# Optimization experiments

Measured on AMD Instinct MI355X. Metric: run time of the kernel, lower is better.

Reference implementation:

```python
import jax, jax.numpy as jnp
import numpy as np

EPS = 1e-5

def _conv3x3(x, w, b):
    # NCHW, OIHW, 3x3 stride 1 pad 1
    y = jax.lax.conv_general_dilated(x, w, window_strides=(1, 1),
                                     padding=((1, 1), (1, 1)),
                                     dimension_numbers=('NCHW', 'OIHW', 'NCHW'))
    return y + b[None, :, None, None]

def _pool_upsample(x, k):
    # adaptive avg pool to (H/k, W/k) then nearest block-upsample back
    B, C, H, W = x.shape
    p = x.reshape(B, C, H // k, k, W // k, k).mean(axis=(3, 5))
    return jnp.repeat(jnp.repeat(p, k, axis=2), k, axis=3)

def setup_inputs() -> dict:
    key = jax.random.key(0)
    ks = jax.random.split(key, 12)
    B, C, H, W = 32, 8, 300, 300
    d = {
        'x': jax.random.normal(ks[0], (B, C, H, W), jnp.float32),
        'w5': jax.random.normal(ks[1], (8, 16, 3, 3), jnp.float32) * 0.1,
        'b5': jnp.zeros((8,), jnp.float32),
        'w10': jax.random.normal(ks[2], (8, 16, 3, 3), jnp.float32) * 0.1,
        'b10': jnp.zeros((8,), jnp.float32),
        'w15': jax.random.normal(ks[3], (8, 16, 3, 3), jnp.float32) * 0.1,
        'b15': jnp.zeros((8,), jnp.float32),
        'gw': jax.random.normal(ks[4], (8, 24, 3, 3), jnp.float32) * 0.1,
        'gb': jnp.zeros((8,), jnp.float32),
        'mw': jax.random.normal(ks[5], (8, 24, 3, 3), jnp.float32) * 0.1,
        'mb': jnp.zeros((8,), jnp.float32),
        'gamma': jnp.ones((8,), jnp.float32),
        'beta': jnp.zeros((8,), jnp.float32),
    }
    return d

def reference(x, w5, b5, w10, b10, w15, b15, gw, gb, mw, mb, gamma, beta):
    up5 = _pool_upsample(x, 5)    # [B,8,300,300]
    up10 = _pool_upsample(x, 10)
    up15 = _pool_upsample(x, 15)
    c5 = _conv3x3(jnp.concatenate([x, up5], axis=1), w5, b5)
    c10 = _conv3x3(jnp.concatenate([x, up10], axis=1), w10, b10)
    c15 = _conv3x3(jnp.concatenate([x, up15], axis=1), w15, b15)
    g_in = jnp.concatenate([c5, c10, c15], axis=1)  # [B,24,H,W]
    # gated conv, activation=None: conv(g_in) * sigmoid(mask_conv(g_in))
    y = _conv3x3(g_in, gw, gb) * jax.nn.sigmoid(_conv3x3(g_in, mw, mb))
    # batch norm (training-mode batch stats, biased var, as torch default)
    mean = y.mean(axis=(0, 2, 3), keepdims=True)
    var = ((y - mean) ** 2).mean(axis=(0, 2, 3), keepdims=True)
    y = (y - mean) * jax.lax.rsqrt(var + EPS)
    return y * gamma[None, :, None, None] + beta[None, :, None, None]
```

## Files before the change

### kernel.cpp

```cpp
#include <hip/hip_runtime.h>
#include <math.h>

typedef __bf16 bfrag __attribute__((ext_vector_type(8)));
typedef __bf16 bf16x4 __attribute__((ext_vector_type(4)));
typedef __bf16 bf16x8 __attribute__((ext_vector_type(8)));
typedef float f32x4 __attribute__((ext_vector_type(4)));

#define BN 32
#define HH 300
#define WW 300
#define HW 90000
#define NPX (BN * HW)

#define GX 10
#define GY 19
#define CPX 612
#define XPX 720
#define CWSTRIDE 4896

#define P5I_BYTE_OFF   0
#define P10I_BYTE_OFF  1843200
#define P15I_BYTE_OFF  2304000
#define CWB_BYTE_OFF   2508800
#define GWB_BYTE_OFF   2524160
#define STAT_BYTE_OFF  2531328
#define SS_BYTE_OFF    2539520
#define XBF_BYTE_OFF   2539584
#define XBF_END        (XBF_BYTE_OFF + (size_t)NPX * 16)

#define XU4_OFF   0
#define P5_OFF4   11520
#define P10_OFF4  12160
#define P15_OFF4  12400
#define CW4_OFF   12592
#define LDS4_SIZE 41968

__device__ __forceinline__ short f2bf(float f) {
    union { float f; unsigned u; } v;
    v.f = f;
    unsigned r = v.u + 0x7FFF + ((v.u >> 16) & 1);
    return (short)(r >> 16);
}

__device__ __forceinline__ float bf2f(unsigned short s) {
    union { unsigned u; float f; } v;
    v.u = ((unsigned)s) << 16;
    return v.f;
}

__device__ __forceinline__ void setup_body(int gid, int gstride,
                                           const float* __restrict__ w5,
                                           const float* __restrict__ w10,
                                           const float* __restrict__ w15,
                                           const float* __restrict__ gw,
                                           const float* __restrict__ mw,
                                           short* __restrict__ cBg,
                                           short* __restrict__ gBg,
                                           double* __restrict__ stats) {
    for (int idx = gid; idx < 7680; idx += gstride) {
        int s = idx / 2560, rem = idx % 2560;
        int n = rem / 160, r2 = rem % 160;
        int tap = r2 / 16, ci = r2 % 16;
        float v = 0.f;
        if (n < 8 && tap < 9) {
            const float* W = (s == 0) ? w5 : ((s == 1) ? w10 : w15);
            v = W[(n * 16 + ci) * 9 + tap];
        }
        cBg[idx] = f2bf(v);
    }
    for (int idx = gid; idx < 3584; idx += gstride) {
        int n = idx / 224, r2 = idx % 224;
        int blk = r2 / 8, cj = r2 % 8;
        float v = 0.f;
        if (blk < 27) {
            int tap = blk / 3, ci24 = (blk % 3) * 8 + cj;
            if (n < 8) v = gw[(n * 24 + ci24) * 9 + tap];
            else       v = mw[((n - 8) * 24 + ci24) * 9 + tap];
        }
        gBg[idx] = f2bf(v);
    }
    for (int idx = gid; idx < 16 * 64; idx += gstride) stats[idx] = 0.0;
}

__global__ void k_setup(const float* __restrict__ w5, const float* __restrict__ w10,
                        const float* __restrict__ w15, const float* __restrict__ gw,
                        const float* __restrict__ mw, short* __restrict__ cBg,
                        short* __restrict__ gBg, double* __restrict__ stats) {
    setup_body(threadIdx.x, 256, w5, w10, w15, gw, mw, cBg, gBg, stats);
}

__global__ __launch_bounds__(256) void k_xbf(const float* __restrict__ x,
                                             unsigned short* __restrict__ xbf,
                                             const float* __restrict__ w5,
                                             const float* __restrict__ w10,
                                             const float* __restrict__ w15,
                                             const float* __restrict__ gw,
                                             const float* __restrict__ mw,
                                             short* __restrict__ cBg,
                                             short* __restrict__ gBg,
                                             double* __restrict__ stats) {
    const int b = blockIdx.y;
    const int px = blockIdx.x * 256 + threadIdx.x;
    if (px < HW) {
        const float* xp = x + (size_t)b * 8 * HW + px;
        bf16x8 pk;
#pragma unroll
        for (int ch = 0; ch < 8; ch++) pk[ch] = (__bf16)xp[(size_t)ch * HW];
        *(bf16x8*)&xbf[((size_t)b * HW + px) * 8] = pk;
    }
    if (blockIdx.y == 0 && blockIdx.x < 16) {
        int gid = blockIdx.x * 256 + threadIdx.x;
        setup_body(gid, 4096, w5, w10, w15, gw, mw, cBg, gBg, stats);
    }
}

__global__ __launch_bounds__(256) void k_poolAll(const unsigned short* __restrict__ xbf,
                                                 unsigned short* __restrict__ p5i,
                                                 unsigned short* __restrict__ p10i,
                                                 unsigned short* __restrict__ p15i) {
    __shared__ __align__(16) short xt[900 * 8];
    __shared__ float p5t[36][8];
    const int b = blockIdx.y;
    const int bi = blockIdx.x / 10, bj = blockIdx.x % 10;
    const int t = threadIdx.x;
    for (int idx = t; idx < 900; idx += 256) {
        int r = idx / 30, c = idx - r * 30;
        *(uint4*)&xt[idx * 8] =
            *(const uint4*)&xbf[((size_t)b * HW + (bi * 30 + r) * WW + bj * 30 + c) * 8];
    }
    __syncthreads();
    if (t < 36) {
        int pi = t / 6, pj = t - (t / 6) * 6;
        float s[8] = {0.f, 0.f, 0.f, 0.f, 0.f, 0.f, 0.f, 0.f};
#pragma unroll
        for (int u = 0; u < 5; u++)
#pragma unroll
            for (int v = 0; v < 5; v++) {
                bf16x8 vv = *(const bf16x8*)&xt[((pi * 5 + u) * 30 + pj * 5 + v) * 8];
#pragma unroll
                for (int ch = 0; ch < 8; ch++) s[ch] += (float)vv[ch];
            }
        bf16x8 pk;
#pragma unroll
        for (int ch = 0; ch < 8; ch++) {
            float av = s[ch] * 0.04f;
            p5t[t][ch] = av;
            pk[ch] = (__bf16)av;
        }
        *(bf16x8*)&p5i[((size_t)b * 3600 + (bi * 6 + pi) * 60 + bj * 6 + pj) * 8] = pk;
    }
    __syncthreads();
    if (t < 9) {
        int pi = t / 3, pj = t - (t / 3) * 3;
        bf16x8 pk;
#pragma unroll
        for (int ch = 0; ch < 8; ch++) {
            float s = p5t[(2 * pi) * 6 + 2 * pj][ch] + p5t[(2 * pi) * 6 + 2 * pj + 1][ch] +
                      p5t[(2 * pi + 1) * 6 + 2 * pj][ch] + p5t[(2 * pi + 1) * 6 + 2 * pj + 1][ch];
            pk[ch] = (__bf16)(s * 0.25f);
        }
        *(bf16x8*)&p10i[((size_t)b * 900 + (bi * 3 + pi) * 30 + bj * 3 + pj) * 8] = pk;
    } else if (t < 13) {
        int i2 = t - 9;
        int pi = i2 >> 1, pj = i2 & 1;
        bf16x8 pk;
#pragma unroll
        for (int ch = 0; ch < 8; ch++) {
            float s = 0.f;
#pragma unroll
            for (int u = 0; u < 3; u++)
#pragma unroll
                for (int v = 0; v < 3; v++) s += p5t[(3 * pi + u) * 6 + 3 * pj + v][ch];
            pk[ch] = (__bf16)(s * (1.f / 9.f));
        }
        *(bf16x8*)&p15i[((size_t)b * 400 + (bi * 2 + pi) * 20 + bj * 2 + pj) * 8] = pk;
    }
}

template <int K, int PCOLS>
__device__ __forceinline__ void c_phase3(char* LDSp, int cwOff, int patchOff,
                                         const unsigned short* __restrict__ cBs,
                                         const float* __restrict__ bias,
                                         int pr0, int pc0,
                                         int r0, int c0, int lane, int wid, bool edge) {
    constexpr int T0[5] = {0, 2, 4, 6, 8};
    constexpr int T1[5] = {1, 3, 5, 7, 8};
    const int n = lane & 15, quad = lane >> 4;
    const int qh = quad >> 1, ql = quad & 1;
    bfrag wfr[5];
#pragma unroll
    for (int km = 0; km < 5; km++) {
        int tapw = km * 2 + qh;
        wfr[km] = *(const bfrag*)&cBs[(n * 10 + tapw) * 16 + ql * 8];
    }
    const int srow = patchOff - pr0 * (PCOLS * 16);
    const int scol = -(pc0 << 4);
    float bO[4];
#pragma unroll
    for (int r = 0; r < 4; r++) bO[r] = bias[(quad & 1) * 4 + r];

    for (int g = wid; g < 39; g += 4) {
        int px = g * 16 + n;
        if (px > 611) px = 611;
        int rp = (int)((unsigned)px / 34u);
        int cp = px - rp * 34;
        int xb = (rp * 36 + cp) * 16;
        int rowB[3], colB[3];
#pragma unroll
        for (int d = 0; d < 3; d++) {
            rowB[d] = (int)(((unsigned)(r0 - 2 + rp + d + K) / (unsigned)K) * (PCOLS * 16)) + srow;
            colB[d] = (int)(((unsigned)(c0 - 2 + cp + d + K) / (unsigned)K) << 4) + scol;
        }
        f32x4 acc = {0.f, 0.f, 0.f, 0.f};
#pragma unroll
        for (int km = 0; km < 5; km++) {
            int au0 = rowB[T0[km] / 3] + colB[T0[km] % 3];
            int au1 = rowB[T1[km] / 3] + colB[T1[km] % 3];
            int ax0 = xb + ((T0[km] / 3) * 36 + (T0[km] % 3)) * 16;
            int ax1 = xb + ((T1[km] / 3) * 36 + (T1[km] % 3)) * 16;
            int au = qh ? au1 : au0;
            int ax = qh ? ax1 : ax0;
            int ad = ql ? au : ax;
            acc = __builtin_amdgcn_mfma_f32_16x16x32_bf16(
                wfr[km], *(const bfrag*)(LDSp + ad), acc, 0, 0, 0);
        }
        if (quad < 2) {
            bf16x4 pk;
#pragma unroll
            for (int r = 0; r < 4; r++) pk[r] = (__bf16)(acc[r] + bO[r]);
            if (edge) {
                int ra = r0 - 1 + rp, ca = c0 - 1 + cp;
                if (ra < 0 || ra >= HH || ca < 0 || ca >= WW) {
#pragma unroll
                    for (int r = 0; r < 4; r++) pk[r] = (__bf16)0.f;
                }
            }
            *(bf16x4*)(LDSp + cwOff + px * 16 + quad * 8) = pk;
        }
    }
}

__global__ __launch_bounds__(256, 3) void k_fused4(
    const unsigned short* __restrict__ xbf,
    const unsigned short* __restrict__ p5i, const unsigned short* __restrict__ p10i,
    const unsigned short* __restrict__ p15i,
    const unsigned short* __restrict__ cBg, const unsigned short* __restrict__ gBg,
    const float* __restrict__ b5, const float* __restrict__ b10, const float* __restrict__ b15,
    const float* __restrict__ gb, const float* __restrict__ mb,
    float* __restrict__ out, double* __restrict__ stats) {
    __shared__ __align__(16) char LDS[LDS4_SIZE];

    const int b = blockIdx.z;
    const int r0 = blockIdx.y * 16, c0 = blockIdx.x * 32;
    const int t = threadIdx.x, lane = t & 63, wid = t >> 6;
    const bool edge = (blockIdx.x == 0) | (blockIdx.x == GX - 1) |
                      (blockIdx.y == 0) | (blockIdx.y == GY - 1);

    const int pr0_5 = (r0 + 3) / 5, pc0_5 = (c0 + 3) / 5;
    const int pr0_10 = (r0 + 8) / 10, pc0_10 = (c0 + 8) / 10;
    const int pr0_15 = (r0 + 13) / 15, pc0_15 = (c0 + 13) / 15;

#pragma unroll
    for (int it = 0; it < 3; it++) {
        int idx = t + 256 * it;
        if (idx < XPX) {
            int i = idx / 36, j = idx - i * 36;
            int ra = r0 - 2 + i, ca = c0 - 2 + j;
            uint4 v = {0u, 0u, 0u, 0u};
            if (ra >= 0 && ra < HH && ca >= 0 && ca < WW)
                v = *(const uint4*)&xbf[((size_t)b * HW + ra * WW + ca) * 8];
            *(uint4*)(LDS + XU4_OFF + idx * 16) = v;
        }
    }
    if (t < 67) {
        const unsigned short* src;
        int off;
        bool valid;
        if (t < 40) {
            int a = t >> 3, cc = t & 7;
            int ci = pr0_5 - 1 + a, cj = pc0_5 - 1 + cc;
            valid = (ci >= 0) && (ci < 60) && (cj >= 0) && (cj < 60);
            src = p5i + ((size_t)b * 3600 + ci * 60 + cj) * 8;
            off = P5_OFF4 + t * 16;
        } else if (t < 55) {
            int i2 = t - 40;
            int a = i2 / 5, cc = i2 % 5;
            int ci = pr0_10 - 1 + a, cj = pc0_10 - 1 + cc;
            valid = (ci >= 0) && (ci < 30) && (cj >= 0) && (cj < 30);
            src = p10i + ((size_t)b * 900 + ci * 30 + cj) * 8;
            off = P10_OFF4 + i2 * 16;
        } else {
            int i2 = t - 55;
            int a = i2 >> 2, cc = i2 & 3;
            int ci = pr0_15 - 1 + a, cj = pc0_15 - 1 + cc;
            valid = (ci >= 0) && (ci < 20) && (cj >= 0) && (cj < 20);
            src = p15i + ((size_t)b * 400 + ci * 20 + cj) * 8;
            off = P15_OFF4 + i2 * 16;
        }
        uint4 v = {0u, 0u, 0u, 0u};
        if (valid) v = *(const uint4*)src;
        *(uint4*)(LDS + off) = v;
    }
    __syncthreads();

    c_phase3<5, 8>(LDS, CW4_OFF,          P5_OFF4,  cBg,        b5,  pr0_5,  pc0_5,  r0, c0, lane, wid, edge);
    c_phase3<10, 5>(LDS, CW4_OFF + 9792,  P10_OFF4, cBg + 2560, b10, pr0_10, pc0_10, r0, c0, lane, wid, edge);
    c_phase3<15, 4>(LDS, CW4_OFF + 19584, P15_OFF4, cBg + 5120, b15, pr0_15, pc0_15, r0, c0, lane, wid, edge);
    __syncthreads();

    const int n = lane & 15, quad = lane >> 4;
    bfrag gfr[7];
    int goff[7];
#pragma unroll
    for (int km = 0; km < 7; km++) {
        int blkw = km * 4 + quad;
        int blka = (blkw > 26) ? 26 : blkw;
        gfr[km] = *(const bfrag*)&gBg[(n * 28 + blkw) * 8];
        int tap = blka / 3, cig = blka - tap * 3;
        goff[km] = cig * 9792 + ((tap / 3) * 34 + tap % 3) * 16;
    }
    float gO[4], mO[4];
#pragma unroll
    for (int r = 0; r < 4; r++) {
        gO[r] = gb[(quad & 1) * 4 + r];
        mO[r] = mb[(quad & 1) * 4 + r];
    }
    float ls[4] = {0.f, 0.f, 0.f, 0.f}, ls2[4] = {0.f, 0.f, 0.f, 0.f};

    for (int g = wid; g < 32; g += 4) {
        int px = g * 16 + n;
        int rr = px >> 5, cc = px & 31;
        int off0 = CW4_OFF + (rr * 34 + cc) * 16;
        f32x4 acc = {0.f, 0.f, 0.f, 0.f};
#pragma unroll
        for (int km = 0; km < 7; km++)
            acc = __builtin_amdgcn_mfma_f32_16x16x32_bf16(
                gfr[km], *(const bfrag*)(LDS + off0 + goff[km]), acc, 0, 0, 0);
        int ra = r0 + rr, ca = c0 + cc;
        bool wr = !edge || (ra < HH && ca < WW);
#pragma unroll
        for (int reg = 0; reg < 4; reg++) {
            float val;
            if (quad < 2) val = acc[reg] + gO[reg];
            else          val = __builtin_amdgcn_rcpf(1.f + __expf(-(acc[reg] + mO[reg])));
            float other = __shfl_xor(val, 32);
            if (quad < 2 && wr) {
                float y = val * other;
                int ch = quad * 4 + reg;
                out[(size_t)(b * 8 + ch) * HW + (size_t)ra * WW + ca] = y;
                ls[reg] += y;
                ls2[reg] += y * y;
            }
        }
    }
#pragma unroll
    for (int m = 1; m < 16; m <<= 1) {
#pragma unroll
        for (int r = 0; r < 4; r++) {
            ls[r] += __shfl_xor(ls[r], m);
            ls2[r] += __shfl_xor(ls2[r], m);
        }
    }
    if (n == 0 && quad < 2) {
        int hash = (blockIdx.x + GX * blockIdx.y + GX * GY * blockIdx.z) & 63;
#pragma unroll
        for (int r = 0; r < 4; r++) {
            atomicAdd(&stats[(quad * 4 + r) * 64 + hash], (double)ls[r]);
            atomicAdd(&stats[(8 + quad * 4 + r) * 64 + hash], (double)ls2[r]);
        }
    }
}

__global__ void k_pool5(const float* __restrict__ x, unsigned short* __restrict__ p5i) {
    int id = blockIdx.x * 256 + threadIdx.x;
    int bc = id / 3600, cell = id % 3600;
    int b = bc >> 3, c = bc & 7;
    int pi = cell / 60, pj = cell % 60;
    const float* rp = x + (size_t)bc * HW + pi * 5 * WW + pj * 5;
    float s = 0.f;
#pragma unroll
    for (int u = 0; u < 5; u++)
#pragma unroll
        for (int v = 0; v < 5; v++) s += rp[u * WW + v];
    p5i[((size_t)b * 3600 + cell) * 8 + c] = (unsigned short)f2bf(s * 0.04f);
}

__global__ void k_poolD(const unsigned short* __restrict__ p5i,
                        unsigned short* __restrict__ p10i,
                        unsigned short* __restrict__ p15i) {
    int id = blockIdx.x * 256 + threadIdx.x;
    if (id < 230400) {
        int bc = id / 900, cell = id % 900;
        int b = bc >> 3, c = bc & 7;
        int pi = cell / 30, pj = cell % 30;
        const unsigned short* base = p5i + ((size_t)b * 3600) * 8 + c;
        float s = bf2f(base[((2 * pi) * 60 + 2 * pj) * 8]) +
                  bf2f(base[((2 * pi) * 60 + 2 * pj + 1) * 8]) +
                  bf2f(base[((2 * pi + 1) * 60 + 2 * pj) * 8]) +
                  bf2f(base[((2 * pi + 1) * 60 + 2 * pj + 1) * 8]);
        p10i[((size_t)b * 900 + cell) * 8 + c] = (unsigned short)f2bf(s * 0.25f);
    } else if (id < 332800) {
        int id2 = id - 230400;
        int bc = id2 / 400, cell = id2 % 400;
        int b = bc >> 3, c = bc & 7;
        int pi = cell / 20, pj = cell % 20;
        const unsigned short* base = p5i + ((size_t)b * 3600) * 8 + c;
        float s = 0.f;
#pragma unroll
        for (int u = 0; u < 3; u++)
#pragma unroll
            for (int v = 0; v < 3; v++)
                s += bf2f(base[((3 * pi + u) * 60 + 3 * pj + v) * 8]);
        p15i[((size_t)b * 400 + cell) * 8 + c] = (unsigned short)f2bf(s * (1.f / 9.f));
    }
}

template <int K, int PW>
__device__ __forceinline__ void up_load(const unsigned short* __restrict__ pooled,
                                        int b, int r0, int c0, int t, uint4* v) {
#pragma unroll
    for (int it = 0; it < 3; it++) {
        int idx = t + 256 * it;
        uint4 val = {0u, 0u, 0u, 0u};
        if (idx < XPX) {
            int i = idx / 36, j = idx - i * 36;
            int ra = r0 - 2 + i, ca = c0 - 2 + j;
            if (ra >= 0 && ra < HH && ca >= 0 && ca < WW) {
                int pi = (int)((unsigned)ra / K);
                int pj = (int)((unsigned)ca / K);
                val = *(const uint4*)&pooled[((size_t)b * (PW * PW) + pi * PW + pj) * 8];
            }
        }
        v[it] = val;
    }
}

__device__ __forceinline__ void up_store(short* xuU, int t, const uint4* v) {
#pragma unroll
    for (int it = 0; it < 3; it++) {
        int idx = t + 256 * it;
        if (idx < XPX) *(uint4*)&xuU[idx * 8] = v[it];
    }
}

__device__ __forceinline__ void c_phase(const short* xuX, const short* xuU,
                                        short* cwP,
                                        const unsigned short* __restrict__ cBs,
                                        const float* __restrict__ bias,
                                        int r0, int c0, int lane, int wid, bool edge) {
    const int n = lane & 15, quad = lane >> 4;
    const int qh = quad >> 1, ql = quad & 1;
    const short* xbase = ql ? xuU : xuX;
    bfrag wfr[5];
    int dpoff[5];
#pragma unroll
    for (int km = 0; km < 5; km++) {
        int tapw = km * 2 + qh;
        int tapa = (tapw > 8) ? 8 : tapw;
        wfr[km] = *(const bfrag*)&cBs[(n * 10 + tapw) * 16 + ql * 8];
        dpoff[km] = ((tapa / 3) * 36 + tapa % 3) * 8;
    }
    float bO[4];
#pragma unroll
    for (int r = 0; r < 4; r++) bO[r] = bias[(quad & 1) * 4 + r];

    for (int g = wid; g < 39; g += 4) {
        int px = g * 16 + n;
        if (px > 611) px = 611;
        int rp = (int)((unsigned)px / 34u);
        int cp = px - rp * 34;
        int pb = (rp * 36 + cp) * 8;
        f32x4 acc = {0.f, 0.f, 0.f, 0.f};
#pragma unroll
        for (int km = 0; km < 5; km++)
            acc = __builtin_amdgcn_mfma_f32_16x16x32_bf16(
                wfr[km], *(const bfrag*)&xbase[pb + dpoff[km]], acc, 0, 0, 0);
        if (quad < 2) {
            bf16x4 pk;
#pragma unroll
            for (int r = 0; r < 4; r++) pk[r] = (__bf16)(acc[r] + bO[r]);
            if (edge) {
                int ra = r0 - 1 + rp, ca = c0 - 1 + cp;
                if (ra < 0 || ra >= HH || ca < 0 || ca >= WW) {
#pragma unroll
                    for (int r = 0; r < 4; r++) pk[r] = (__bf16)0.f;
                }
            }
            *(bf16x4*)&cwP[px * 8 + quad * 4] = pk;
        }
    }
}

__global__ __launch_bounds__(256, 3) void k_fused_fb(
    const float* __restrict__ x,
    const unsigned short* __restrict__ p5i, const unsigned short* __restrict__ p10i,
    const unsigned short* __restrict__ p15i,
    const unsigned short* __restrict__ cBg, const unsigned short* __restrict__ gBg,
    const float* __restrict__ b5, const float* __restrict__ b10, const float* __restrict__ b15,
    const float* __restrict__ gb, const float* __restrict__ mb,
    float* __restrict__ out, double* __restrict__ stats) {
    __shared__ __align__(16) short xuX[XPX * 8];
    __shared__ __align__(16) short xuU[XPX * 8];
    __shared__ __align__(16) short cwS[3 * CWSTRIDE];

    const int b = blockIdx.z;
    const int r0 = blockIdx.y * 16, c0 = blockIdx.x * 32;
    const int t = threadIdx.x, lane = t & 63, wid = t >> 6;
    const bool edge = (blockIdx.x == 0) | (blockIdx.x == GX - 1) |
                      (blockIdx.y == 0) | (blockIdx.y == GY - 1);

    uint4 upv[3];
    up_load<5, 60>(p5i, b, r0, c0, t, upv);

    for (int idx = t; idx < 1440; idx += 256) {
        int cp = idx / 360, rem = idx % 360;
        int i = rem / 18, jp = rem % 18;
        int j = 2 * jp;
        int ra = r0 - 2 + i, ca = c0 - 2 + j;
        float2 v0 = {0.f, 0.f}, v1 = {0.f, 0.f};
        if (ra >= 0 && ra < HH && ca >= 0 && ca <= WW - 2) {
            size_t base = ((size_t)(b * 8 + 2 * cp) * HH + ra) * WW + ca;
            v0 = *(const float2*)&x[base];
            v1 = *(const float2*)&x[base + HW];
        }
        unsigned pA = (unsigned short)f2bf(v0.x) | ((unsigned)(unsigned short)f2bf(v1.x) << 16);
        unsigned pB = (unsigned short)f2bf(v0.y) | ((unsigned)(unsigned short)f2bf(v1.y) << 16);
        int px = i * 36 + j;
        *(unsigned*)&xuX[px * 8 + 2 * cp] = pA;
        *(unsigned*)&xuX[(px + 1) * 8 + 2 * cp] = pB;
    }
    up_store(xuU, t, upv);
    __syncthreads();

    c_phase(xuX, xuU, cwS, cBg, b5, r0, c0, lane, wid, edge);
    up_load<10, 30>(p10i, b, r0, c0, t, upv);
    __syncthreads();
    up_store(xuU, t, upv);
    __syncthreads();

    c_phase(xuX, xuU, cwS + CWSTRIDE, cBg + 2560, b10, r0, c0, lane, wid, edge);
    up_load<15, 20>(p15i, b, r0, c0, t, upv);
    __syncthreads();
    up_store(xuU, t, upv);
    __syncthreads();

    c_phase(xuX, xuU, cwS + 2 * CWSTRIDE, cBg + 5120, b15, r0, c0, lane, wid, edge);
    __syncthreads();

    const int n = lane & 15, quad = lane >> 4;
    bfrag gfr[7];
    int goff[7];
#pragma unroll
    for (int km = 0; km < 7; km++) {
        int blkw = km * 4 + quad;
        int blka = (blkw > 26) ? 26 : blkw;
        gfr[km] = *(const bfrag*)&gBg[(n * 28 + blkw) * 8];
        int tap = blka / 3, cig = blka - tap * 3;
        goff[km] = cig * CWSTRIDE + ((tap / 3) * 34 + tap % 3) * 8;
    }
    float gO[4], mO[4];
#pragma unroll
    for (int r = 0; r < 4; r++) {
        gO[r] = gb[(quad & 1) * 4 + r];
        mO[r] = mb[(quad & 1) * 4 + r];
    }
    float ls[4] = {0.f, 0.f, 0.f, 0.f}, ls2[4] = {0.f, 0.f, 0.f, 0.f};

    for (int g = wid; g < 32; g += 4) {
        int px = g * 16 + n;
        int rr = px >> 5, cc = px & 31;
        int off0 = (rr * 34 + cc) * 8;
        f32x4 acc = {0.f, 0.f, 0.f, 0.f};
#pragma unroll
        for (int km = 0; km < 7; km++)
            acc = __builtin_amdgcn_mfma_f32_16x16x32_bf16(
                gfr[km], *(const bfrag*)&cwS[off0 + goff[km]], acc, 0, 0, 0);
        int ra = r0 + rr, ca = c0 + cc;
        bool wr = !edge || (ra < HH && ca < WW);
#pragma unroll
        for (int reg = 0; reg < 4; reg++) {
            float val;
            if (quad < 2) val = acc[reg] + gO[reg];
            else          val = __builtin_amdgcn_rcpf(1.f + __expf(-(acc[reg] + mO[reg])));
            float other = __shfl_xor(val, 32);
            if (quad < 2 && wr) {
                float y = val * other;
                int ch = quad * 4 + reg;
                out[(size_t)(b * 8 + ch) * HW + (size_t)ra * WW + ca] = y;
                ls[reg] += y;
                ls2[reg] += y * y;
            }
        }
    }
#pragma unroll
    for (int m = 1; m < 16; m <<= 1) {
#pragma unroll
        for (int r = 0; r < 4; r++) {
            ls[r] += __shfl_xor(ls[r], m);
            ls2[r] += __shfl_xor(ls2[r], m);
        }
    }
    if (n == 0 && quad < 2) {
        int hash = (blockIdx.x + GX * blockIdx.y + GX * GY * blockIdx.z) & 63;
#pragma unroll
        for (int r = 0; r < 4; r++) {
            atomicAdd(&stats[(quad * 4 + r) * 64 + hash], (double)ls[r]);
            atomicAdd(&stats[(8 + quad * 4 + r) * 64 + hash], (double)ls2[r]);
        }
    }
}

__global__ void k_stats(const double* __restrict__ stats, const float* __restrict__ gamma,
                        const float* __restrict__ beta, float* __restrict__ ss) {
    __shared__ double red[16][16];
    int t = threadIdx.x;
    int row = t >> 4, col = t & 15;
    double s = stats[row * 64 + col] + stats[row * 64 + col + 16] +
               stats[row * 64 + col + 32] + stats[row * 64 + col + 48];
    red[row][col] = s;
    __syncthreads();
    if (t < 16) {
        double tot = 0.0;
#pragma unroll
        for (int i = 0; i < 16; i++) tot += red[t][i];
        red[t][0] = tot;
    }
    __syncthreads();
    if (t < 8) {
        double N = (double)NPX;
        double mean = red[t][0] / N;
        double var = red[8 + t][0] / N - mean * mean;
        double scale = (double)gamma[t] / sqrt(var + 1e-5);
        ss[t] = (float)scale;
        ss[8 + t] = (float)((double)beta[t] - mean * scale);
    }
}

__global__ void k_norm(float* __restrict__ out, const float* __restrict__ ss) {
    int i = blockIdx.x * 256 + threadIdx.x;
    if (i < (BN * 8 * HW) / 4) {
        int plane = (i * 4) / HW;
        int ch = plane & 7;
        float sc = ss[ch], sh = ss[8 + ch];
        float4* p = (float4*)out + i;
        float4 v = *p;
        v.x = v.x * sc + sh;
        v.y = v.y * sc + sh;
        v.z = v.z * sc + sh;
        v.w = v.w * sc + sh;
        *p = v;
    }
}

extern "C" void kernel_launch(void* const* d_in, const int* in_sizes, int n_in,
                              void* d_out, int out_size, void* d_ws, size_t ws_size,
                              hipStream_t stream) {
    const float* x = (const float*)d_in[0];
    const float* w5 = (const float*)d_in[1];
    const float* b5 = (const float*)d_in[2];
    const float* w10 = (const float*)d_in[3];
    const float* b10 = (const float*)d_in[4];
    const float* w15 = (const float*)d_in[5];
    const float* b15 = (const float*)d_in[6];
    const float* gw = (const float*)d_in[7];
    const float* gb = (const float*)d_in[8];
    const float* mw = (const float*)d_in[9];
    const float* mb = (const float*)d_in[10];
    const float* gamma = (const float*)d_in[11];
    const float* beta = (const float*)d_in[12];
    float* out = (float*)d_out;

    unsigned short* p5i = (unsigned short*)((char*)d_ws + P5I_BYTE_OFF);
    unsigned short* p10i = (unsigned short*)((char*)d_ws + P10I_BYTE_OFF);
    unsigned short* p15i = (unsigned short*)((char*)d_ws + P15I_BYTE_OFF);
    short* cBg = (short*)((char*)d_ws + CWB_BYTE_OFF);
    short* gBg = (short*)((char*)d_ws + GWB_BYTE_OFF);
    double* stats = (double*)((char*)d_ws + STAT_BYTE_OFF);
    float* ss = (float*)((char*)d_ws + SS_BYTE_OFF);
    unsigned short* xbf = (unsigned short*)((char*)d_ws + XBF_BYTE_OFF);

    dim3 grid(GX, GY, BN);
    if (ws_size >= XBF_END) {
        k_xbf<<<dim3(352, 32), 256, 0, stream>>>(x, xbf, w5, w10, w15, gw, mw,
                                                 cBg, gBg, stats);
        k_poolAll<<<dim3(100, 32), 256, 0, stream>>>(xbf, p5i, p10i, p15i);
        k_fused4<<<grid, 256, 0, stream>>>(xbf, p5i, p10i, p15i,
                                           (const unsigned short*)cBg, (const unsigned short*)gBg,
                                           b5, b10, b15, gb, mb, out, stats);
    } else {
        k_setup<<<1, 256, 0, stream>>>(w5, w10, w15, gw, mw, cBg, gBg, stats);
        k_pool5<<<3600, 256, 0, stream>>>(x, p5i);
        k_poolD<<<1300, 256, 0, stream>>>(p5i, p10i, p15i);
        k_fused_fb<<<grid, 256, 0, stream>>>(x, p5i, p10i, p15i,
                                             (const unsigned short*)cBg, (const unsigned short*)gBg,
                                             b5, b10, b15, gb, mb, out, stats);
    }
    k_stats<<<1, 256, 0, stream>>>(stats, gamma, beta, ss);
    k_norm<<<(BN * 8 * HW / 4 + 255) / 256, 256, 0, stream>>>(out, ss);
}
```

Baseline: 383.6 us.

## Fuse bf16 conversion with pooling, use LUT addressing, merge stats into norm

Merges the x-to-bf16 transpose kernel and the pooling kernel into one prep kernel. It reads fp32 x tiles into LDS once, writes the packed bf16 copy and computes all pools from the fp32 tile, so the bf16 intermediate is never re-read. In the fused conv kernel, per-pixel divisions for the upsample row and column offsets are replaced by small LDS lookup tables built once per block. The single-block stats kernel and the normalize kernel are merged into one grid-stride kernel where every block recomputes the scale and shift. This saves launches and traffic at the cost of redundant stats reduction per block and more LDS use.

Measured after the change: 396.4 us. 1.03x slower.

```diff
diff --git a/kernel.cpp b/kernel.cpp
--- a/kernel.cpp
+++ b/kernel.cpp
@@ -89,57 +89,52 @@
     setup_body(threadIdx.x, 256, w5, w10, w15, gw, mw, cBg, gBg, stats);
 }
 
-__global__ __launch_bounds__(256) void k_xbf(const float* __restrict__ x,
-                                             unsigned short* __restrict__ xbf,
-                                             const float* __restrict__ w5,
-                                             const float* __restrict__ w10,
-                                             const float* __restrict__ w15,
-                                             const float* __restrict__ gw,
-                                             const float* __restrict__ mw,
-                                             short* __restrict__ cBg,
-                                             short* __restrict__ gBg,
-                                             double* __restrict__ stats) {
-    const int b = blockIdx.y;
-    const int px = blockIdx.x * 256 + threadIdx.x;
-    if (px < HW) {
-        const float* xp = x + (size_t)b * 8 * HW + px;
-        bf16x8 pk;
-#pragma unroll
-        for (int ch = 0; ch < 8; ch++) pk[ch] = (__bf16)xp[(size_t)ch * HW];
-        *(bf16x8*)&xbf[((size_t)b * HW + px) * 8] = pk;
-    }
-    if (blockIdx.y == 0 && blockIdx.x < 16) {
-        int gid = blockIdx.x * 256 + threadIdx.x;
-        setup_body(gid, 4096, w5, w10, w15, gw, mw, cBg, gBg, stats);
-    }
-}
-
-__global__ __launch_bounds__(256) void k_poolAll(const unsigned short* __restrict__ xbf,
+__global__ __launch_bounds__(256) void k_prepAll(const float* __restrict__ x,
+                                                 unsigned short* __restrict__ xbf,
                                                  unsigned short* __restrict__ p5i,
                                                  unsigned short* __restrict__ p10i,
-                                                 unsigned short* __restrict__ p15i) {
-    __shared__ __align__(16) short xt[900 * 8];
+                                                 unsigned short* __restrict__ p15i,
+                                                 const float* __restrict__ w5,
+                                                 const float* __restrict__ w10,
+                                                 const float* __restrict__ w15,
+                                                 const float* __restrict__ gw,
+                                                 const float* __restrict__ mw,
+                                                 short* __restrict__ cBg,
+                                                 short* __restrict__ gBg,
+                                                 double* __restrict__ stats) {
+    __shared__ float tf[8][900];
     __shared__ float p5t[36][8];
-    const int b = blockIdx.y;
+    const int b = blockIdx.y, t = threadIdx.x;
     const int bi = blockIdx.x / 10, bj = blockIdx.x % 10;
-    const int t = threadIdx.x;
+    const float* xb0 = x + (size_t)b * 8 * HW + (bi * 30) * WW + bj * 30;
+
+    for (int idx = t; idx < 3600; idx += 256) {
+        int ch = idx / 450, rem = idx % 450;
+        int r = rem / 15, c2 = rem % 15;
+        float2 v = *(const float2*)&xb0[(size_t)ch * HW + r * WW + 2 * c2];
+        tf[ch][r * 30 + 2 * c2] = v.x;
+        tf[ch][r * 30 + 2 * c2 + 1] = v.y;
+    }
+    if (blockIdx.y == 0 && blockIdx.x < 16)
+        setup_body(blockIdx.x * 256 + t, 4096, w5, w10, w15, gw, mw, cBg, gBg, stats);
+    __syncthreads();
+
     for (int idx = t; idx < 900; idx += 256) {
         int r = idx / 30, c = idx - r * 30;
-        *(uint4*)&xt[idx * 8] =
-            *(const uint4*)&xbf[((size_t)b * HW + (bi * 30 + r) * WW + bj * 30 + c) * 8];
-    }
-    __syncthreads();
+        bf16x8 pk;
+#pragma unroll
+        for (int ch = 0; ch < 8; ch++) pk[ch] = (__bf16)tf[ch][idx];
+        *(bf16x8*)&xbf[((size_t)b * HW + (bi * 30 + r) * WW + bj * 30 + c) * 8] = pk;
+    }
     if (t < 36) {
         int pi = t / 6, pj = t - (t / 6) * 6;
         float s[8] = {0.f, 0.f, 0.f, 0.f, 0.f, 0.f, 0.f, 0.f};
 #pragma unroll
-        for (int u = 0; u < 5; u++)
-#pragma unroll
-            for (int v = 0; v < 5; v++) {
-                bf16x8 vv = *(const bf16x8*)&xt[((pi * 5 + u) * 30 + pj * 5 + v) * 8];
-#pragma unroll
-                for (int ch = 0; ch < 8; ch++) s[ch] += (float)vv[ch];
-            }
+        for (int ch = 0; ch < 8; ch++)
+#pragma unroll
+            for (int u = 0; u < 5; u++)
+#pragma unroll
+                for (int v = 0; v < 5; v++) s[ch] += tf[ch][(pi * 5 + u) * 30 + pj * 5 + v];
         bf16x8 pk;
 #pragma unroll
         for (int ch = 0; ch < 8; ch++) {
@@ -177,11 +172,10 @@
     }
 }
 
-template <int K, int PCOLS>
-__device__ __forceinline__ void c_phase3(char* LDSp, int cwOff, int patchOff,
+__device__ __forceinline__ void c_phase5(char* LDSp, int cwOff,
                                          const unsigned short* __restrict__ cBs,
                                          const float* __restrict__ bias,
-                                         int pr0, int pc0,
+                                         const int* lr, const int* lc,
                                          int r0, int c0, int lane, int wid, bool edge) {
     constexpr int T0[5] = {0, 2, 4, 6, 8};
     constexpr int T1[5] = {1, 3, 5, 7, 8};
@@ -193,8 +187,6 @@
         int tapw = km * 2 + qh;
         wfr[km] = *(const bfrag*)&cBs[(n * 10 + tapw) * 16 + ql * 8];
     }
-    const int srow = patchOff - pr0 * (PCOLS * 16);
-    const int scol = -(pc0 << 4);
     float bO[4];
 #pragma unroll
     for (int r = 0; r < 4; r++) bO[r] = bias[(quad & 1) * 4 + r];
@@ -205,21 +197,21 @@
         int rp = (int)((unsigned)px / 34u);
         int cp = px - rp * 34;
         int xb = (rp * 36 + cp) * 16;
-        int rowB[3], colB[3];
-#pragma unroll
-        for (int d = 0; d < 3; d++) {
-            rowB[d] = (int)(((unsigned)(r0 - 2 + rp + d + K) / (unsigned)K) * (PCOLS * 16)) + srow;
-            colB[d] = (int)(((unsigned)(c0 - 2 + cp + d + K) / (unsigned)K) << 4) + scol;
-        }
+        int lr0 = lr[rp], lr1 = lr[rp + 1], lr2 = lr[rp + 2];
+        int lc0 = lc[cp], lc1 = lc[cp + 1], lc2 = lc[cp + 2];
         f32x4 acc = {0.f, 0.f, 0.f, 0.f};
 #pragma unroll
         for (int km = 0; km < 5; km++) {
-            int au0 = rowB[T0[km] / 3] + colB[T0[km] % 3];
-            int au1 = rowB[T1[km] / 3] + colB[T1[km] % 3];
-            int ax0 = xb + ((T0[km] / 3) * 36 + (T0[km] % 3)) * 16;
-            int ax1 = xb + ((T1[km] / 3) * 36 + (T1[km] % 3)) * 16;
-            int au = qh ? au1 : au0;
-            int ax = qh ? ax1 : ax0;
+            constexpr int d0r[5] = {0, 0, 1, 2, 2}, d0c[5] = {0, 2, 1, 0, 2};
+            constexpr int d1r[5] = {0, 1, 1, 2, 2}, d1c[5] = {1, 0, 2, 1, 2};
+            int dr = qh ? d1r[km] : d0r[km];
+            int dc = qh ? d1c[km] : d0c[km];
+            int rA = (dr == 0) ? lr0 : ((dr == 1) ? lr1 : lr2);
+            int cA = (dc == 0) ? lc0 : ((dc == 1) ? lc1 : lc2);
+            int au = rA + cA;
+            int xo = qh ? ((T1[km] / 3) * 36 + T1[km] % 3) * 16
+                        : ((T0[km] / 3) * 36 + T0[km] % 3) * 16;
+            int ax = xb + xo;
             int ad = ql ? au : ax;
             acc = __builtin_amdgcn_mfma_f32_16x16x32_bf16(
                 wfr[km], *(const bfrag*)(LDSp + ad), acc, 0, 0, 0);
@@ -240,7 +232,7 @@
     }
 }
 
-__global__ __launch_bounds__(256, 3) void k_fused4(
+__global__ __launch_bounds__(256, 3) void k_fused5(
     const unsigned short* __restrict__ xbf,
     const unsigned short* __restrict__ p5i, const unsigned short* __restrict__ p10i,
     const unsigned short* __restrict__ p15i,
@@ -249,6 +241,8 @@
     const float* __restrict__ gb, const float* __restrict__ mb,
     float* __restrict__ out, double* __restrict__ stats) {
     __shared__ __align__(16) char LDS[LDS4_SIZE];
+    __shared__ int lutR[3][20];
+    __shared__ int lutC[3][36];
 
     const int b = blockIdx.z;
     const int r0 = blockIdx.y * 16, c0 = blockIdx.x * 32;
@@ -301,11 +295,26 @@
         if (valid) v = *(const uint4*)src;
         *(uint4*)(LDS + off) = v;
     }
-    __syncthreads();
-
-    c_phase3<5, 8>(LDS, CW4_OFF,          P5_OFF4,  cBg,        b5,  pr0_5,  pc0_5,  r0, c0, lane, wid, edge);
-    c_phase3<10, 5>(LDS, CW4_OFF + 9792,  P10_OFF4, cBg + 2560, b10, pr0_10, pc0_10, r0, c0, lane, wid, edge);
-    c_phase3<15, 4>(LDS, CW4_OFF + 19584, P15_OFF4, cBg + 5120, b15, pr0_15, pc0_15, r0, c0, lane, wid, edge);
+    if (t < 168) {
+        int set = t / 56, e = t % 56;
+        int K = (set == 0) ? 5 : ((set == 1) ? 10 : 15);
+        int PC = (set == 0) ? 8 : ((set == 1) ? 5 : 4);
+        int pOff = (set == 0) ? P5_OFF4 : ((set == 1) ? P10_OFF4 : P15_OFF4);
+        int pr = (set == 0) ? pr0_5 : ((set == 1) ? pr0_10 : pr0_15);
+        int pc = (set == 0) ? pc0_5 : ((set == 1) ? pc0_10 : pc0_15);
+        if (e < 20)
+            lutR[set][e] = (int)((unsigned)(r0 - 2 + e + K) / (unsigned)K) * (PC * 16)
+                           + pOff - pr * (PC * 16);
+        else {
+            int j = e - 20;
+            lutC[set][j] = (int)((unsigned)(c0 - 2 + j + K) / (unsigned)K) * 16 - pc * 16;
+        }
+    }
+    __syncthreads();
+
+    c_phase5(LDS, CW4_OFF,         cBg,        b5,  lutR[0], lutC[0], r0, c0, lane, wid, edge);
+    c_phase5(LDS, CW4_OFF + 9792,  cBg + 2560, b10, lutR[1], lutC[1], r0, c0, lane, wid, edge);
+    c_phase5(LDS, CW4_OFF + 19584, cBg + 5120, b15, lutR[2], lutC[2], r0, c0, lane, wid, edge);
     __syncthreads();
 
     const int n = lane & 15, quad = lane >> 4;
@@ -368,6 +377,48 @@
             atomicAdd(&stats[(quad * 4 + r) * 64 + hash], (double)ls[r]);
             atomicAdd(&stats[(8 + quad * 4 + r) * 64 + hash], (double)ls2[r]);
         }
+    }
+}
+
+__global__ __launch_bounds__(256) void k_normS(float* __restrict__ out,
+                                               const double* __restrict__ stats,
+                                               const float* __restrict__ gamma,
+                                               const float* __restrict__ beta) {
+    __shared__ double red[16][16];
+    __shared__ float ssl[16];
+    int t = threadIdx.x;
+    int row = t >> 4, col = t & 15;
+    double s = stats[row * 64 + col] + stats[row * 64 + col + 16] +
+               stats[row * 64 + col + 32] + stats[row * 64 + col + 48];
+    red[row][col] = s;
+    __syncthreads();
+    if (t < 16) {
+        double tot = 0.0;
+#pragma unroll
+        for (int i = 0; i < 16; i++) tot += red[t][i];
+        red[t][0] = tot;
+    }
+    __syncthreads();
+    if (t < 8) {
+        double N = (double)NPX;
+        double mean = red[t][0] / N;
+        double var = red[8 + t][0] / N - mean * mean;
+        double scale = (double)gamma[t] / sqrt(var + 1e-5);
+        ssl[t] = (float)scale;
+        ssl[8 + t] = (float)((double)beta[t] - mean * scale);
+    }
+    __syncthreads();
+    const int total = (BN * 8 * HW) / 4;
+    for (int i = blockIdx.x * 256 + t; i < total; i += 2048 * 256) {
+        int ch = (i / 22500) & 7;
+        float sc = ssl[ch], sh = ssl[8 + ch];
+        float4* p = (float4*)out + i;
+        float4 v = *p;
+        v.x = v.x * sc + sh;
+        v.y = v.y * sc + sh;
+        v.z = v.z * sc + sh;
+        v.w = v.w * sc + sh;
+        *p = v;
     }
 }
 
@@ -681,12 +732,13 @@
 
     dim3 grid(GX, GY, BN);
     if (ws_size >= XBF_END) {
-        k_xbf<<<dim3(352, 32), 256, 0, stream>>>(x, xbf, w5, w10, w15, gw, mw,
-                                                 cBg, gBg, stats);
-        k_poolAll<<<dim3(100, 32), 256, 0, stream>>>(xbf, p5i, p10i, p15i);
-        k_fused4<<<grid, 256, 0, stream>>>(xbf, p5i, p10i, p15i,
+        k_prepAll<<<dim3(100, 32), 256, 0, stream>>>(x, xbf, p5i, p10i, p15i,
+                                                     w5, w10, w15, gw, mw,
+                                                     cBg, gBg, stats);
+        k_fused5<<<grid, 256, 0, stream>>>(xbf, p5i, p10i, p15i,
                                            (const unsigned short*)cBg, (const unsigned short*)gBg,
                                            b5, b10, b15, gb, mb, out, stats);
+        k_normS<<<2048, 256, 0, stream>>>(out, stats, gamma, beta);
     } else {
         k_setup<<<1, 256, 0, stream>>>(w5, w10, w15, gw, mw, cBg, gBg, stats);
         k_pool5<<<3600, 256, 0, stream>>>(x, p5i);
@@ -694,7 +746,7 @@
         k_fused_fb<<<grid, 256, 0, stream>>>(x, p5i, p10i, p15i,
                                              (const unsigned short*)cBg, (const unsigned short*)gBg,
                                              b5, b10, b15, gb, mb, out, stats);
-    }
-    k_stats<<<1, 256, 0, stream>>>(stats, gamma, beta, ss);
-    k_norm<<<(BN * 8 * HW / 4 + 255) / 256, 256, 0, stream>>>(out, ss);
-}
+        k_stats<<<1, 256, 0, stream>>>(stats, gamma, beta, ss);
+        k_norm<<<(BN * 8 * HW / 4 + 255) / 256, 256, 0, stream>>>(out, ss);
+    }
+}
```
